# Kernel optimization log

Measured on AMD Instinct MI355X. Metric: run time of the kernel, lower is better.

## Reference

```python
import jax, jax.numpy as jnp
import numpy as np

KUP = 5       # reassembly kernel size
DELTA = 2     # upsample ratio
KENC = 3      # encoder conv kernel size
CM = 64       # compressed channels
INC = 256
OUTC = 256


def conv2d(x, w, b, pad):
    # x: (N,C,H,W), w: (O,I,kh,kw)
    y = jax.lax.conv_general_dilated(
        x, w, window_strides=(1, 1), padding=[(pad, pad), (pad, pad)],
        dimension_numbers=("NCHW", "OIHW", "NCHW"))
    return y + b[None, :, None, None]


def pixel_shuffle(x, r):
    # torch semantics: channel c*r^2 + i*r + j -> (c, h*r+i, w*r+j)
    N, Cr2, H, W = x.shape
    C = Cr2 // (r * r)
    x = x.reshape(N, C, r, r, H, W)
    x = x.transpose(0, 1, 4, 2, 5, 3)
    return x.reshape(N, C, H * r, W * r)


def setup_inputs() -> dict:
    key = jax.random.key(0)
    ks = jax.random.split(key, 7)
    N, H, W = 4, 64, 64
    x = jax.random.normal(ks[0], (N, INC, H, W), dtype=jnp.float32)
    w_down = jax.random.normal(ks[1], (CM, INC, 1, 1), dtype=jnp.float32) * 0.05
    b_down = jnp.zeros((CM,), jnp.float32)
    enc_out = DELTA * DELTA * KUP * KUP  # 100
    w_enc = jax.random.normal(ks[2], (enc_out, CM, KENC, KENC), dtype=jnp.float32) * 0.05
    b_enc = jnp.zeros((enc_out,), jnp.float32)
    w_out = jax.random.normal(ks[3], (OUTC, INC, 1, 1), dtype=jnp.float32) * 0.05
    b_out = jnp.zeros((OUTC,), jnp.float32)
    return {"in_tensor": x, "w_down": w_down, "b_down": b_down,
            "w_enc": w_enc, "b_enc": b_enc, "w_out": w_out, "b_out": b_out}


def reference(in_tensor, w_down, b_down, w_enc, b_enc, w_out, b_out):
    N, C, H, W = in_tensor.shape
    k2, d2 = KUP * KUP, DELTA * DELTA

    # --- kernel prediction branch ---
    k = conv2d(in_tensor, w_down, b_down, 0)          # (N, Cm, H, W)
    k = conv2d(k, w_enc, b_enc, KENC // 2)            # (N, k2*d2, H, W)
    # pixel_shuffle + per-upsampled-pixel softmax over Kup^2, fused:
    # channel index = kup_idx * delta^2 + subpixel_idx (torch pixel_shuffle layout)
    k = k.reshape(N, k2, d2, H, W)
    k = jax.nn.softmax(k, axis=1)
    kern = k.transpose(0, 3, 4, 1, 2)                 # (N, H, W, k2, d2)

    # --- feature reassembly ---
    pad = KUP // 2
    xp = jnp.pad(in_tensor, ((0, 0), (0, 0), (pad, pad), (pad, pad)))
    # (N, C, H, W, Kup^2); k index = kh*Kup + kw, matching torch unfold order
    patches = jnp.stack(
        [xp[:, :, i:i + H, j:j + W] for i in range(KUP) for j in range(KUP)],
        axis=-1)

    out = jnp.einsum("nchwk,nhwkd->nhwcd", patches, kern)  # (N,H,W,C,d2)
    out = out.reshape(N, H, W, C * d2).transpose(0, 3, 1, 2)  # (N, C*d2, H, W)
    out = pixel_shuffle(out, DELTA)                   # (N, C, H*delta, W*delta)

    return conv2d(out, w_out, b_out, 0)               # (N, outC, H*delta, W*delta)
```

## Files before the change

### kernel.cpp

```cpp
#include <hip/hip_runtime.h>
#include <hip/hip_bf16.h>


namespace {
constexpr int kN = 4, kH = 64, kW = 64, kINC = 256, kCM = 64;
constexpr int kENC = 100, kH2 = 128, kW2 = 128, kOUTC = 256;
constexpr int kHW = kH * kW;
constexpr int kHW2 = kH2 * kW2;
constexpr int kPadW = 66;
constexpr int kTImg = kPadW * kPadW * kCM;
constexpr int kZPad = 68;
constexpr int kZImg = kZPad * kZPad * kOUTC;
constexpr int kXP = 264;
constexpr int kPrepRepackEnc = 9 * 7 * 2 * 512;
constexpr int kPrepRepackWoz = 8 * 20 * 512;
constexpr int kPrepHaloZ = 4 * 528 * 8;
constexpr int kPrepHaloD = 4 * 260 * 8;
constexpr int kPrepTotal = kPrepRepackEnc + kPrepRepackWoz + kPrepHaloZ + kPrepHaloD;
constexpr int kPrepBlocks = (kPrepTotal + 255) / 256;
}

typedef __attribute__((ext_vector_type(8))) short short8;
typedef __attribute__((ext_vector_type(4))) float floatx4;

static __device__ __forceinline__ unsigned short bf16bits(float f) {
  __hip_bfloat16 h = __float2bfloat16(f);
  return *(unsigned short*)&h;
}

static __device__ __forceinline__ float bf2f(unsigned short u) {
  union { unsigned int i; float f; } c;
  c.i = ((unsigned int)u) << 16;
  return c.f;
}

__global__ __launch_bounds__(256) void k_prep(
    const float* __restrict__ we, unsigned short* __restrict__ Aswz,
    const float* __restrict__ wd, const float* __restrict__ wo,
    unsigned short* __restrict__ Awoz,
    __hip_bfloat16* __restrict__ zT, __hip_bfloat16* __restrict__ downT) {
  const int t = blockIdx.x * 256 + threadIdx.x;
  if (t < kPrepRepackEnc) {
    const int e = t;
    const int j = e & 7, lane = (e >> 3) & 63, kh = (e >> 9) & 1, tm = e >> 10;
    const int mt = tm % 7, tap = tm / 7;
    const int o = mt * 16 + (lane & 15);
    const int ci = kh * 32 + ((lane >> 4) & 3) * 8 + j;
    const float v = (o < kENC) ? we[(size_t)o * 576 + ci * 9 + tap] : 0.f;
    Aswz[e] = bf16bits(v);
  } else if (t < kPrepRepackEnc + kPrepRepackWoz) {
    const int e = t - kPrepRepackEnc;
    const int j = e & 7, lane = (e >> 3) & 63;
    const int rest = e >> 9;
    const int mt = rest % 20, ks = rest / 20;
    const int r = mt * 16 + (lane & 15);
    const int k = ks * 32 + (lane >> 4) * 8 + j;
    const float v = (r < kCM) ? wd[(size_t)r * kINC + k]
                              : wo[(size_t)(r - kCM) * kINC + k];
    Awoz[e] = bf16bits(v);
  } else if (t < kPrepTotal) {
    const int u0 = t - (kPrepRepackEnc + kPrepRepackWoz);
    if (u0 < kPrepHaloZ) {
      const int chunk = u0 & 7, rest = u0 >> 3;
      const int i = rest % 528, n = rest / 528;
      int r, c;
      if (i < 272) { r = i / 68; if (r >= 2) r += 64; c = i % 68; }
      else { const int j = i - 272; r = 2 + (j >> 2); const int cc = j & 3; c = (cc < 2) ? cc : cc + 64; }
      float4* p = (float4*)((char*)zT
                  + ((size_t)n * kZImg + ((size_t)r * kZPad + c) * kOUTC) * 2) + chunk;
      *p = make_float4(0.f, 0.f, 0.f, 0.f);
    } else {
      const int u = u0 - kPrepHaloZ;
      const int chunk = u & 7, rest = u >> 3;
      const int i = rest % 260, n = rest / 260;
      int r, c;
      if (i < 132) { r = (i / 66) ? 65 : 0; c = i % 66; }
      else { const int j = i - 132; r = 1 + (j >> 1); c = (j & 1) ? 65 : 0; }
      float4* p = (float4*)((char*)downT
                  + ((size_t)n * kTImg + ((size_t)r * kPadW + c) * kCM) * 2) + chunk;
      *p = make_float4(0.f, 0.f, 0.f, 0.f);
    }
  }
}

__global__ __launch_bounds__(256) void k_dzmfma(
    const float* __restrict__ x, const unsigned short* __restrict__ Awoz,
    const float* __restrict__ bd, __hip_bfloat16* __restrict__ downT,
    __hip_bfloat16* __restrict__ zT) {
  const int b = blockIdx.x;
  const int pt = b & 255, n = b >> 8;
  const int wave = threadIdx.x >> 6, lane = threadIdx.x & 63;
  const int col = lane & 15, quad = lane >> 4;
  const int px = pt * 16 + col;
  const int h = px >> 6, w = px & 63;

  __shared__ unsigned short xlds[16 * kXP];

  {
    const float* xb = x + (size_t)n * kINC * kHW + px;
#pragma unroll
    for (int ki = 0; ki < 2; ++ki) {
      const int ks = wave * 2 + ki;
      float xv[8];
#pragma unroll
      for (int j = 0; j < 8; ++j)
        xv[j] = xb[(size_t)(ks * 32 + quad * 8 + j) * kHW];
      short8 bf;
#pragma unroll
      for (int j = 0; j < 8; ++j) bf[j] = (short)bf16bits(xv[j]);
      *(short8*)(xlds + col * kXP + ks * 32 + quad * 8) = bf;
    }
  }
  __syncthreads();

  floatx4 acc[5];
#pragma unroll
  for (int m = 0; m < 5; ++m) acc[m] = (floatx4){0.f, 0.f, 0.f, 0.f};

#pragma unroll
  for (int ks = 0; ks < 8; ++ks) {
    const short8 bf = *(const short8*)(xlds + col * kXP + ks * 32 + quad * 8);
#pragma unroll
    for (int m = 0; m < 5; ++m) {
      const int wtile = wave * 5 + m;
      const short8 af = *(const short8*)(
          Awoz + ((size_t)(ks * 20 + wtile) * 64 + lane) * 8);
      acc[m] = __builtin_amdgcn_mfma_f32_16x16x32_bf16(af, bf, acc[m], 0, 0, 0);
    }
  }

#pragma unroll
  for (int m = 0; m < 5; ++m) {
    const int wtile = wave * 5 + m;
    const int r0 = wtile * 16 + quad * 4;
    if (wtile < 4) {
      union { unsigned short u[4]; uint2 v; } pk;
#pragma unroll
      for (int rr = 0; rr < 4; ++rr)
        pk.u[rr] = bf16bits(acc[m][rr] + bd[r0 + rr]);
      __hip_bfloat16* dst = downT + (size_t)n * kTImg
                            + ((h + 1) * kPadW + (w + 1)) * kCM + r0;
      *(uint2*)dst = pk.v;
    } else {
      const int o = r0 - kCM;
      union { unsigned short u[4]; uint2 v; } pk;
#pragma unroll
      for (int rr = 0; rr < 4; ++rr)
        pk.u[rr] = bf16bits(acc[m][rr]);
      __hip_bfloat16* dst = zT + (size_t)n * kZImg
                            + ((h + 2) * kZPad + (w + 2)) * kOUTC + o;
      *(uint2*)dst = pk.v;
    }
  }
}

__global__ __launch_bounds__(256) void k_encmfma(
    const __hip_bfloat16* __restrict__ downT,
    const unsigned short* __restrict__ Aswz,
    const float* __restrict__ be, float* __restrict__ enc) {
  const int b = blockIdx.x;
  const int h = b & 63, mtp = (b >> 6) & 3, n = b >> 8;
  const int wave = threadIdx.x >> 6, lane = threadIdx.x & 63;
  const int w0 = wave << 4;
  const int col = lane & 15, quad = lane >> 4;
  const int mt0 = mtp * 2;
  const bool has2 = (mt0 + 1) < 7;
  const short* dT = (const short*)downT + (size_t)n * kTImg;
  floatx4 acc0 = {0.f, 0.f, 0.f, 0.f}, acc1 = {0.f, 0.f, 0.f, 0.f};
#pragma unroll
  for (int tap = 0; tap < 9; ++tap) {
    const int dh = tap / 3 - 1, dw = tap % 3 - 1;
    const int rowbase = ((h + 1 + dh) * kPadW + (w0 + col + 1 + dw)) * kCM
                        + quad * 8;
#pragma unroll
    for (int kh = 0; kh < 2; ++kh) {
      const short8 bf = *(const short8*)(dT + rowbase + kh * 32);
      const short8 a0 = *(const short8*)(
          Aswz + (((size_t)(tap * 7 + mt0) * 2 + kh) * 64 + lane) * 8);
      acc0 = __builtin_amdgcn_mfma_f32_16x16x32_bf16(a0, bf, acc0, 0, 0, 0);
      if (has2) {
        const short8 a1 = *(const short8*)(
            Aswz + (((size_t)(tap * 7 + mt0 + 1) * 2 + kh) * 64 + lane) * 8);
        acc1 = __builtin_amdgcn_mfma_f32_16x16x32_bf16(a1, bf, acc1, 0, 0, 0);
      }
    }
  }
  const int p = h * kW + w0 + col;
#pragma unroll
  for (int r = 0; r < 4; ++r) {
    const int o = mt0 * 16 + quad * 4 + r;
    if (o < kENC) enc[(size_t)(n * kENC + o) * kHW + p] = acc0[r] + be[o];
  }
  if (has2) {
#pragma unroll
    for (int r = 0; r < 4; ++r) {
      const int o = (mt0 + 1) * 16 + quad * 4 + r;
      if (o < kENC) enc[(size_t)(n * kENC + o) * kHW + p] = acc1[r] + be[o];
    }
  }
}

__global__ __launch_bounds__(256) void k_fused_out(
    const __hip_bfloat16* __restrict__ zT, const float* __restrict__ enc,
    const float* __restrict__ bo, float* __restrict__ out) {
  const int b = blockIdx.x;
  const int pt = b & 255, oh = (b >> 8) & 1, n = b >> 9;
  const int tid = threadIdx.x;
  const int wave = tid >> 6, lane = tid & 63;
  const int h = pt >> 2, w0 = (pt & 3) << 4;
  const int px0 = pt * 16;

  __shared__ float lds[1664 + 4160];
  float* kernLDS = lds;
  float* scr = lds + 1664;

  {
    const int p = tid & 15, chb = tid >> 4;
#pragma unroll
    for (int r = 0; r < 7; ++r) {
      const int ch = r * 16 + chb;
      if (ch < kENC)
        kernLDS[p * 104 + ch] = enc[((size_t)n * kENC + ch) * kHW + px0 + p];
    }
  }
  __syncthreads();

  {
    const int pair = tid >> 2, q = tid & 3;
    const int p = pair >> 2, d = pair & 3;
    float* kb = kernLDS + p * 104 + d;
    const int start = q ? (1 + 6 * q) : 0;
    const int count = q ? 6 : 7;
    float v[7];
    float m = -1e30f;
#pragma unroll
    for (int k = 0; k < 7; ++k)
      if (k < count) { v[k] = kb[(start + k) * 4]; m = fmaxf(m, v[k]); }
    m = fmaxf(m, __shfl_xor(m, 1));
    m = fmaxf(m, __shfl_xor(m, 2));
    float s = 0.f;
#pragma unroll
    for (int k = 0; k < 7; ++k)
      if (k < count) { v[k] = __expf(v[k] - m); s += v[k]; }
    s += __shfl_xor(s, 1);
    s += __shfl_xor(s, 2);
    const float inv = 1.f / s;
#pragma unroll
    for (int k = 0; k < 7; ++k)
      if (k < count) kb[(start + k) * 4] = v[k] * inv;
  }
  __syncthreads();

  const int oc = lane & 15, pxi = lane >> 4;
  const int px_l = wave * 4 + pxi;
  const int w = w0 + px_l;
  const int o_l = oc * 4;
  const float* kp = kernLDS + px_l * 104;
  const int ol2 = tid >> 2, q2 = tid & 3;

#pragma unroll
  for (int ogi = 0; ogi < 2; ++ogi) {
    const int og = oh * 2 + ogi;

    const unsigned short* zb =
        (const unsigned short*)zT + (size_t)n * kZImg + og * 64 + o_l;
    float acc[4][4] = {};
#pragma unroll
    for (int tap = 0; tap < 25; ++tap) {
      const int kh = tap / 5, kw = tap % 5;
      const ushort4 zu = *(const ushort4*)(
          zb + ((size_t)(h + kh) * kZPad + (w + kw)) * kOUTC);
      const float4 kf = *(const float4*)(kp + tap * 4);
      const float zx = bf2f(zu.x), zy = bf2f(zu.y), zz = bf2f(zu.z), zw = bf2f(zu.w);
      acc[0][0] += zx * kf.x; acc[0][1] += zx * kf.y; acc[0][2] += zx * kf.z; acc[0][3] += zx * kf.w;
      acc[1][0] += zy * kf.x; acc[1][1] += zy * kf.y; acc[1][2] += zy * kf.z; acc[1][3] += zy * kf.w;
      acc[2][0] += zz * kf.x; acc[2][1] += zz * kf.y; acc[2][2] += zz * kf.z; acc[2][3] += zz * kf.w;
      acc[3][0] += zw * kf.x; acc[3][1] += zw * kf.y; acc[3][2] += zw * kf.z; acc[3][3] += zw * kf.w;
    }

    __syncthreads();
#pragma unroll
    for (int oi = 0; oi < 4; ++oi)
#pragma unroll
      for (int d = 0; d < 4; ++d)
        scr[(o_l + oi) * 65 + px_l * 4 + d] = acc[oi][d];
    __syncthreads();

    const int o = og * 64 + ol2;
    const float bias = bo[o];
    const float* Trow = scr + ol2 * 65;
#pragma unroll
    for (int i = 0; i < 2; ++i) {
      float* row = out + ((size_t)(n * kOUTC + o) * kH2 + (2 * h + i)) * kW2 + 2 * w0;
#pragma unroll
      for (int s = 0; s < 2; ++s) {
        const int xb_ = s * 16 + q2 * 4;
        float4 v;
        v.x = Trow[((xb_ + 0) >> 1) * 4 + i * 2 + ((xb_ + 0) & 1)] + bias;
        v.y = Trow[((xb_ + 1) >> 1) * 4 + i * 2 + ((xb_ + 1) & 1)] + bias;
        v.z = Trow[((xb_ + 2) >> 1) * 4 + i * 2 + ((xb_ + 2) & 1)] + bias;
        v.w = Trow[((xb_ + 3) >> 1) * 4 + i * 2 + ((xb_ + 3) & 1)] + bias;
        *(float4*)(row + xb_) = v;
      }
    }
  }
}

extern "C" void kernel_launch(void* const* d_in, const int* in_sizes, int n_in,
                              void* d_out, int out_size, void* d_ws, size_t ws_size,
                              hipStream_t stream) {
  const float* x  = (const float*)d_in[0];
  const float* wd = (const float*)d_in[1];
  const float* bd = (const float*)d_in[2];
  const float* we = (const float*)d_in[3];
  const float* be = (const float*)d_in[4];
  const float* wo = (const float*)d_in[5];
  const float* bo = (const float*)d_in[6];
  float* out = (float*)d_out;

  float* enc = (float*)d_ws;
  __hip_bfloat16* zT = (__hip_bfloat16*)(enc + 1638400);
  __hip_bfloat16* downT = zT + (size_t)kN * kZImg;
  unsigned short* Aswz  = (unsigned short*)(downT + (size_t)kN * kTImg);
  unsigned short* Awoz  = Aswz + 64512;

  k_prep<<<kPrepBlocks, 256, 0, stream>>>(we, Aswz, wd, wo, Awoz, zT, downT);
  k_dzmfma<<<1024, 256, 0, stream>>>(x, Awoz, bd, downT, zT);
  k_encmfma<<<1024, 256, 0, stream>>>(downT, Aswz, be, enc);
  k_fused_out<<<2048, 256, 0, stream>>>(zT, enc, bo, out);
}
```

Baseline: 141.4 us.

## Fuse encoder conv into reassembly kernel, staging downT slab in LDS

Merges the 3x3 encoder MFMA conv into the reassembly/output kernel. Each block now computes the 100 kernel logits for its 16 pixels from a downT halo slab staged in LDS, and writes them straight into the shared kernel buffer. This removes the global enc round trip and one launch. In exchange, each block now handles all four output-channel groups, so the grid halves to 1024 blocks and per-block serial work grows.

```diff
diff --git a/kernel.cpp b/kernel.cpp
--- a/kernel.cpp
+++ b/kernel.cpp
@@ -154,73 +154,71 @@
   }
 }
 
-__global__ __launch_bounds__(256) void k_encmfma(
+__global__ __launch_bounds__(256) void k_tail(
+    const __hip_bfloat16* __restrict__ zT,
     const __hip_bfloat16* __restrict__ downT,
-    const unsigned short* __restrict__ Aswz,
-    const float* __restrict__ be, float* __restrict__ enc) {
-  const int b = blockIdx.x;
-  const int h = b & 63, mtp = (b >> 6) & 3, n = b >> 8;
-  const int wave = threadIdx.x >> 6, lane = threadIdx.x & 63;
-  const int w0 = wave << 4;
-  const int col = lane & 15, quad = lane >> 4;
-  const int mt0 = mtp * 2;
-  const bool has2 = (mt0 + 1) < 7;
-  const short* dT = (const short*)downT + (size_t)n * kTImg;
-  floatx4 acc0 = {0.f, 0.f, 0.f, 0.f}, acc1 = {0.f, 0.f, 0.f, 0.f};
-#pragma unroll
-  for (int tap = 0; tap < 9; ++tap) {
-    const int dh = tap / 3 - 1, dw = tap % 3 - 1;
-    const int rowbase = ((h + 1 + dh) * kPadW + (w0 + col + 1 + dw)) * kCM
-                        + quad * 8;
-#pragma unroll
-    for (int kh = 0; kh < 2; ++kh) {
-      const short8 bf = *(const short8*)(dT + rowbase + kh * 32);
-      const short8 a0 = *(const short8*)(
-          Aswz + (((size_t)(tap * 7 + mt0) * 2 + kh) * 64 + lane) * 8);
-      acc0 = __builtin_amdgcn_mfma_f32_16x16x32_bf16(a0, bf, acc0, 0, 0, 0);
-      if (has2) {
-        const short8 a1 = *(const short8*)(
-            Aswz + (((size_t)(tap * 7 + mt0 + 1) * 2 + kh) * 64 + lane) * 8);
-        acc1 = __builtin_amdgcn_mfma_f32_16x16x32_bf16(a1, bf, acc1, 0, 0, 0);
-      }
-    }
-  }
-  const int p = h * kW + w0 + col;
-#pragma unroll
-  for (int r = 0; r < 4; ++r) {
-    const int o = mt0 * 16 + quad * 4 + r;
-    if (o < kENC) enc[(size_t)(n * kENC + o) * kHW + p] = acc0[r] + be[o];
-  }
-  if (has2) {
-#pragma unroll
-    for (int r = 0; r < 4; ++r) {
-      const int o = (mt0 + 1) * 16 + quad * 4 + r;
-      if (o < kENC) enc[(size_t)(n * kENC + o) * kHW + p] = acc1[r] + be[o];
-    }
-  }
-}
-
-__global__ __launch_bounds__(256) void k_fused_out(
-    const __hip_bfloat16* __restrict__ zT, const float* __restrict__ enc,
+    const unsigned short* __restrict__ Aswz, const float* __restrict__ be,
     const float* __restrict__ bo, float* __restrict__ out) {
   const int b = blockIdx.x;
-  const int pt = b & 255, oh = (b >> 8) & 1, n = b >> 9;
+  const int pt = b & 255, n = b >> 8;
   const int tid = threadIdx.x;
   const int wave = tid >> 6, lane = tid & 63;
   const int h = pt >> 2, w0 = (pt & 3) << 4;
-  const int px0 = pt * 16;
 
   __shared__ float lds[1664 + 4160];
   float* kernLDS = lds;
+  unsigned short* slab = (unsigned short*)(lds + 1664);
   float* scr = lds + 1664;
 
   {
-    const int p = tid & 15, chb = tid >> 4;
-#pragma unroll
-    for (int r = 0; r < 7; ++r) {
-      const int ch = r * 16 + chb;
-      if (ch < kENC)
-        kernLDS[p * 104 + ch] = enc[((size_t)n * kENC + ch) * kHW + px0 + p];
+    const unsigned short* dTg = (const unsigned short*)downT + (size_t)n * kTImg;
+#pragma unroll
+    for (int it = 0; it < 2; ++it) {
+      const int idx = it * 256 + tid;
+      if (idx < 432) {
+        const int chunk = idx & 7, rowcol = idx >> 3;
+        const int row = rowcol / 18, c = rowcol % 18;
+        const short8 v = *(const short8*)(
+            dTg + (((size_t)(h + row) * kPadW) + (w0 + c)) * kCM + chunk * 8);
+        *(short8*)(slab + (chunk * 54 + row * 18 + c) * 8) = v;
+      }
+    }
+  }
+  __syncthreads();
+
+  {
+    const int col = lane & 15, quad = lane >> 4;
+    const int mt0 = wave * 2;
+    const bool has2 = (mt0 + 1) < 7;
+    floatx4 acc0 = {0.f, 0.f, 0.f, 0.f}, acc1 = {0.f, 0.f, 0.f, 0.f};
+#pragma unroll
+    for (int tap = 0; tap < 9; ++tap) {
+      const int dh = tap / 3, dw = tap % 3;
+#pragma unroll
+      for (int kh = 0; kh < 2; ++kh) {
+        const short8 bf = *(const short8*)(
+            slab + ((kh * 4 + quad) * 54 + dh * 18 + (col + dw)) * 8);
+        const short8 a0 = *(const short8*)(
+            Aswz + (((size_t)(tap * 7 + mt0) * 2 + kh) * 64 + lane) * 8);
+        acc0 = __builtin_amdgcn_mfma_f32_16x16x32_bf16(a0, bf, acc0, 0, 0, 0);
+        if (has2) {
+          const short8 a1 = *(const short8*)(
+              Aswz + (((size_t)(tap * 7 + mt0 + 1) * 2 + kh) * 64 + lane) * 8);
+          acc1 = __builtin_amdgcn_mfma_f32_16x16x32_bf16(a1, bf, acc1, 0, 0, 0);
+        }
+      }
+    }
+#pragma unroll
+    for (int r = 0; r < 4; ++r) {
+      const int o = mt0 * 16 + quad * 4 + r;
+      if (o < kENC) kernLDS[col * 104 + o] = acc0[r] + be[o];
+    }
+    if (has2) {
+#pragma unroll
+      for (int r = 0; r < 4; ++r) {
+        const int o = (mt0 + 1) * 16 + quad * 4 + r;
+        if (o < kENC) kernLDS[col * 104 + o] = acc1[r] + be[o];
+      }
     }
   }
   __syncthreads();
@@ -259,9 +257,7 @@
   const int ol2 = tid >> 2, q2 = tid & 3;
 
 #pragma unroll
-  for (int ogi = 0; ogi < 2; ++ogi) {
-    const int og = oh * 2 + ogi;
-
+  for (int og = 0; og < 4; ++og) {
     const unsigned short* zb =
         (const unsigned short*)zT + (size_t)n * kZImg + og * 64 + o_l;
     float acc[4][4] = {};
@@ -326,6 +322,5 @@
 
   k_prep<<<kPrepBlocks, 256, 0, stream>>>(we, Aswz, wd, wo, Awoz, zT, downT);
   k_dzmfma<<<1024, 256, 0, stream>>>(x, Awoz, bd, downT, zT);
-  k_encmfma<<<1024, 256, 0, stream>>>(downT, Aswz, be, enc);
-  k_fused_out<<<2048, 256, 0, stream>>>(zT, enc, bo, out);
-}
+  k_tail<<<1024, 256, 0, stream>>>(zT, downT, Aswz, be, bo, out);
+}
```

Measured after the change: 144.2 us. About the same (+1.9%).
